# Kernel optimization log

Hardware: AMD Instinct MI355X
Metric: run time of the kernel (lower is better)

The kernel has to match this reference:

```python
import jax, jax.numpy as jnp
import numpy as np

LAM = 10.0          # lam_val from __init__ (cp.Constant)
N_ITERS = 100       # fixed FISTA iterations; converges to QP solution (kappa ~ 1+16*LAM)


def _dtd(v):
    """Apply D^T D where D is the (n-2, n) second-difference operator, along last axis."""
    d = v[..., 2:] - 2.0 * v[..., 1:-1] + v[..., :-2]            # D v, shape (..., n-2)
    pad = [(0, 0)] * (v.ndim - 1) + [(2, 2)]
    dp = jnp.pad(d, pad)                                          # zero-pad for adjoint
    return dp[..., 2:] - 2.0 * dp[..., 1:-1] + dp[..., :-2]      # D^T d, shape (..., n)


def _solve_rows(y):
    """Batched QP:  min ||y - x||^2 + LAM * ||diff(x, 2)||^2  s.t.  0 <= x <= y,
    solved independently along the last axis via projected accelerated gradient (FISTA).
    Hessian/2 = I + LAM * D^T D, lambda_max(D^T D) <= 16 -> Lipschitz L = 2*(1 + 16*LAM).
    """
    step = 1.0 / (2.0 * (1.0 + 16.0 * LAM))
    proj = lambda v: jnp.clip(v, 0.0, y)   # box projection onto [0, y]
    x0 = proj(y)

    def body(i, carry):
        x, z, t = carry
        g = 2.0 * (z - y) + (2.0 * LAM) * _dtd(z)
        x_new = proj(z - step * g)
        t_new = 0.5 * (1.0 + jnp.sqrt(1.0 + 4.0 * t * t))
        z_new = x_new + ((t - 1.0) / t_new) * (x_new - x)
        return (x_new, z_new, t_new)

    x, _, _ = jax.lax.fori_loop(0, N_ITERS, body, (x0, x0, jnp.float32(1.0)))
    return x


def setup_inputs() -> dict:
    key = jax.random.key(0)
    # Batch of images in [0,1] (like normalized MNIST); constraint 0 <= x <= y is feasible.
    data = jax.random.uniform(key, (32, 512, 512), dtype=jnp.float32)
    return {"data": data}


def reference(data):
    # Pass 1: denoise each row of each image.
    pass1 = _solve_rows(data)
    # Pass 2: the original call() transposes a numpy VIEW and writes in place, so its
    # "column" pass actually re-solves the SAME rows (with y = pass-1 output) and the
    # final transpose undoes itself. We replicate that exact math.
    pass2 = _solve_rows(pass1)
    b, h, w = pass2.shape
    return pass2.reshape(b, h, w, 1)
```

## Files before the change

kernel.cpp:

```cpp
#include <hip/hip_runtime.h>
#include <math.h>

#define ROW_N 512
#define N_ITERS 100
#define LAMBDA 10.0f

typedef float f2 __attribute__((ext_vector_type(2)));

__device__ __forceinline__ f2 splat(float s) { f2 r; r.x = s; r.y = s; return r; }
__device__ __forceinline__ f2 ffma(f2 a, f2 b, f2 c) {
    return __builtin_elementwise_fma(a, b, c);
}

__global__ void coef_kernel(float* __restrict__ coefs) {
    if (threadIdx.x == 0) {
        float t = 1.0f;
        for (int k = 0; k < N_ITERS; ++k) {
            float t_new = 0.5f * (1.0f + sqrtf(1.0f + 4.0f * t * t));
            coefs[k] = (t - 1.0f) / t_new;
            t = t_new;
        }
    }
}

template <bool USE_TABLE>
__global__ __launch_bounds__(256)
__attribute__((amdgpu_waves_per_eu(2, 8)))
void fista_kernel(
    const float* __restrict__ in, float* __restrict__ out,
    const float* __restrict__ coefs, int n_rows)
{
    const int pid  = (int)((blockIdx.x * 256u + threadIdx.x) >> 6);
    const int lane = (int)(threadIdx.x & 63u);
    const int n_pairs = (n_rows + 1) >> 1;
    if (pid >= n_pairs) return;

    const bool lane_lo = (lane == 0);
    const bool lane_hi = (lane == 63);

    const int r0 = pid * 2;
    const int r1 = (r0 + 1 < n_rows) ? r0 + 1 : r0;
    const float* rowA = in + (size_t)r0 * ROW_N + lane * 8;
    const float* rowB = in + (size_t)r1 * ROW_N + lane * 8;

    const float A = 1.0f / (1.0f + 16.0f * LAMBDA);
    const float B = LAMBDA / (1.0f + 16.0f * LAMBDA);
    const float C = 1.0f - A;
    const f2 Cv = splat(C), Av = splat(A), Bn = splat(-B), M2 = splat(-2.0f);
    const f2 Z2 = splat(0.0f);

    f2 y[8], ay[8], x[8], z[8];
    {
        const float4 a0 = *(const float4*)(rowA);
        const float4 a1 = *(const float4*)(rowA + 4);
        const float4 b0 = *(const float4*)(rowB);
        const float4 b1 = *(const float4*)(rowB + 4);
        y[0].x = a0.x; y[1].x = a0.y; y[2].x = a0.z; y[3].x = a0.w;
        y[4].x = a1.x; y[5].x = a1.y; y[6].x = a1.z; y[7].x = a1.w;
        y[0].y = b0.x; y[1].y = b0.y; y[2].y = b0.z; y[3].y = b0.w;
        y[4].y = b1.x; y[5].y = b1.y; y[6].y = b1.z; y[7].y = b1.w;
    }

    #pragma unroll 1
    for (int pass = 0; pass < 2; ++pass) {
        #pragma unroll
        for (int i = 0; i < 8; ++i) {
            ay[i] = Av * y[i];
            f2 x0;
            x0.x = fminf(fmaxf(y[i].x, 0.0f), y[i].x);
            x0.y = fminf(fmaxf(y[i].y, 0.0f), y[i].y);
            x[i] = x0;
            z[i] = x0;
        }

        f2 zm2, zm1, zp0, zp1;
        zm2.x = __shfl_up(z[6].x, 1);   zm2.y = __shfl_up(z[6].y, 1);
        zm1.x = __shfl_up(z[7].x, 1);   zm1.y = __shfl_up(z[7].y, 1);
        zp0.x = __shfl_down(z[0].x, 1); zp0.y = __shfl_down(z[0].y, 1);
        zp1.x = __shfl_down(z[1].x, 1); zp1.y = __shfl_down(z[1].y, 1);
        float coef, t = 1.0f;
        if (USE_TABLE) coef = coefs[0];
        else           coef = 0.0f;

        #pragma unroll 2
        for (int it = 0; it < N_ITERS; ++it) {
            float coef_next;
            if (USE_TABLE) {
                coef_next = coefs[it + 1 < N_ITERS ? it + 1 : 0];
            } else {
                float t_new = 0.5f + sqrtf(fmaf(t, t, 0.25f));
                coef_next = (t_new - 1.0f) / (0.5f + sqrtf(fmaf(t_new, t_new, 0.25f)));
                t = t_new;
            }

            const f2 cf = splat(coef);
            auto upd = [&](int i, f2 da, f2 db, f2 dc) {
                f2 dtd = ffma(M2, db, da + dc);
                f2 u = ffma(Cv, z[i], ay[i]);
                u = ffma(Bn, dtd, u);
                f2 xn;
                xn.x = __builtin_amdgcn_fmed3f(u.x, 0.0f, y[i].x);
                xn.y = __builtin_amdgcn_fmed3f(u.y, 0.0f, y[i].y);
                z[i] = ffma(cf, xn - x[i], xn);
                x[i] = xn;
            };

            f2 dd2 = ffma(M2, z[1], z[0] + z[2]);
            f2 dd3 = ffma(M2, z[2], z[1] + z[3]);
            f2 dd4 = ffma(M2, z[3], z[2] + z[4]);
            f2 dd5 = ffma(M2, z[4], z[3] + z[5]);
            f2 dd6 = ffma(M2, z[5], z[4] + z[6]);
            f2 dd7 = ffma(M2, z[6], z[5] + z[7]);

            upd(2, dd2, dd3, dd4);
            upd(3, dd3, dd4, dd5);
            upd(4, dd4, dd5, dd6);
            upd(5, dd5, dd6, dd7);

            f2 dd8 = ffma(M2, z[7], z[6] + zp0);
            f2 dd9 = ffma(M2, zp0, z[7] + zp1);
            if (lane_hi) { dd8 = Z2; dd9 = Z2; }

            upd(6, dd6, dd7, dd8);
            upd(7, dd7, dd8, dd9);

            f2 nzm2, nzm1;
            nzm2.x = __shfl_up(z[6].x, 1); nzm2.y = __shfl_up(z[6].y, 1);
            nzm1.x = __shfl_up(z[7].x, 1); nzm1.y = __shfl_up(z[7].y, 1);

            f2 dd0 = ffma(M2, zm1, zm2 + z[0]);
            f2 dd1 = ffma(M2, z[0], zm1 + z[1]);
            if (lane_lo) { dd0 = Z2; dd1 = Z2; }

            upd(0, dd0, dd1, dd2);
            upd(1, dd1, dd2, dd3);

            zp0.x = __shfl_down(z[0].x, 1); zp0.y = __shfl_down(z[0].y, 1);
            zp1.x = __shfl_down(z[1].x, 1); zp1.y = __shfl_down(z[1].y, 1);

            zm2 = nzm2; zm1 = nzm1;
            coef = coef_next;
        }

        #pragma unroll
        for (int i = 0; i < 8; ++i) y[i] = x[i];
    }

    float* orowA = out + (size_t)r0 * ROW_N + lane * 8;
    *(float4*)(orowA)     = make_float4(x[0].x, x[1].x, x[2].x, x[3].x);
    *(float4*)(orowA + 4) = make_float4(x[4].x, x[5].x, x[6].x, x[7].x);
    if (r1 > r0) {
        float* orowB = out + (size_t)r1 * ROW_N + lane * 8;
        *(float4*)(orowB)     = make_float4(x[0].y, x[1].y, x[2].y, x[3].y);
        *(float4*)(orowB + 4) = make_float4(x[4].y, x[5].y, x[6].y, x[7].y);
    }
}

extern "C" void kernel_launch(void* const* d_in, const int* in_sizes, int n_in,
                              void* d_out, int out_size, void* d_ws, size_t ws_size,
                              hipStream_t stream) {
    const float* in = (const float*)d_in[0];
    float* out = (float*)d_out;

    const int total   = in_sizes[0];
    const int n_rows  = total / ROW_N;
    const int n_pairs = (n_rows + 1) >> 1;
    const int waves_per_block = 4;
    const int blocks = (n_pairs + waves_per_block - 1) / waves_per_block;

    if (ws_size >= N_ITERS * sizeof(float)) {
        float* coefs = (float*)d_ws;
        coef_kernel<<<1, 64, 0, stream>>>(coefs);
        fista_kernel<true><<<blocks, 256, 0, stream>>>(in, out, coefs, n_rows);
    } else {
        fista_kernel<false><<<blocks, 256, 0, stream>>>(in, out, nullptr, n_rows);
    }
}
```

Measured before the change: 360.6 us.

## Expand DᵀD stencil into pentadiagonal FMA form and reorder shuffles for overlap

Rewrites each gradient step to apply DᵀD directly as a 5-point pentadiagonal stencil with precomputed coefficients (C-6B, 4B, -B), with boundary-lane coefficients chosen per lane instead of masking intermediate second differences. Edge elements are updated first so the cross-lane shuffles for the next iteration can be issued before the interior updates, hiding shuffle latency. The coefficient table is padded so the per-iteration index clamp can be dropped. The cost is a few extra per-lane constant registers; the reassociated stencil can also change floating-point rounding slightly.

```diff
diff --git a/kernel.cpp b/kernel.cpp
--- a/kernel.cpp
+++ b/kernel.cpp
@@ -3,6 +3,7 @@
 
 #define ROW_N 512
 #define N_ITERS 100
+#define CTAB_N (N_ITERS + 4)
 #define LAMBDA 10.0f
 
 typedef float f2 __attribute__((ext_vector_type(2)));
@@ -15,10 +16,14 @@
 __global__ void coef_kernel(float* __restrict__ coefs) {
     if (threadIdx.x == 0) {
         float t = 1.0f;
-        for (int k = 0; k < N_ITERS; ++k) {
-            float t_new = 0.5f * (1.0f + sqrtf(1.0f + 4.0f * t * t));
-            coefs[k] = (t - 1.0f) / t_new;
-            t = t_new;
+        float c = 0.0f;
+        for (int k = 0; k < CTAB_N; ++k) {
+            if (k < N_ITERS) {
+                float t_new = 0.5f * (1.0f + sqrtf(1.0f + 4.0f * t * t));
+                c = (t - 1.0f) / t_new;
+                t = t_new;
+            }
+            coefs[k] = c;
         }
     }
 }
@@ -46,8 +51,18 @@
     const float A = 1.0f / (1.0f + 16.0f * LAMBDA);
     const float B = LAMBDA / (1.0f + 16.0f * LAMBDA);
     const float C = 1.0f - A;
-    const f2 Cv = splat(C), Av = splat(A), Bn = splat(-B), M2 = splat(-2.0f);
+    const f2 Av = splat(A);
+    const f2 C6 = splat(C - 6.0f * B);
+    const f2 B4 = splat(4.0f * B);
+    const f2 Bm = splat(-B);
     const f2 Z2 = splat(0.0f);
+
+    const f2 cz0   = lane_lo ? splat(C - B)        : C6;
+    const f2 cz1   = lane_lo ? splat(C - 5.0f * B) : C6;
+    const f2 ca_lo = lane_lo ? splat(2.0f * B)     : B4;
+    const f2 cz6   = lane_hi ? splat(C - 5.0f * B) : C6;
+    const f2 cz7   = lane_hi ? splat(C - B)        : C6;
+    const f2 ca_hi = lane_hi ? splat(2.0f * B)     : B4;
 
     f2 y[8], ay[8], x[8], z[8];
     {
@@ -86,7 +101,7 @@
         for (int it = 0; it < N_ITERS; ++it) {
             float coef_next;
             if (USE_TABLE) {
-                coef_next = coefs[it + 1 < N_ITERS ? it + 1 : 0];
+                coef_next = coefs[it + 1];
             } else {
                 float t_new = 0.5f + sqrtf(fmaf(t, t, 0.25f));
                 coef_next = (t_new - 1.0f) / (0.5f + sqrtf(fmaf(t_new, t_new, 0.25f)));
@@ -94,10 +109,7 @@
             }
 
             const f2 cf = splat(coef);
-            auto upd = [&](int i, f2 da, f2 db, f2 dc) {
-                f2 dtd = ffma(M2, db, da + dc);
-                f2 u = ffma(Cv, z[i], ay[i]);
-                u = ffma(Bn, dtd, u);
+            auto fin = [&](int i, f2 u) {
                 f2 xn;
                 xn.x = __builtin_amdgcn_fmed3f(u.x, 0.0f, y[i].x);
                 xn.y = __builtin_amdgcn_fmed3f(u.y, 0.0f, y[i].y);
@@ -105,40 +117,66 @@
                 x[i] = xn;
             };
 
-            f2 dd2 = ffma(M2, z[1], z[0] + z[2]);
-            f2 dd3 = ffma(M2, z[2], z[1] + z[3]);
-            f2 dd4 = ffma(M2, z[3], z[2] + z[4]);
-            f2 dd5 = ffma(M2, z[4], z[3] + z[5]);
-            f2 dd6 = ffma(M2, z[5], z[4] + z[6]);
-            f2 dd7 = ffma(M2, z[6], z[5] + z[7]);
-
-            upd(2, dd2, dd3, dd4);
-            upd(3, dd3, dd4, dd5);
-            upd(4, dd4, dd5, dd6);
-            upd(5, dd5, dd6, dd7);
-
-            f2 dd8 = ffma(M2, z[7], z[6] + zp0);
-            f2 dd9 = ffma(M2, zp0, z[7] + zp1);
-            if (lane_hi) { dd8 = Z2; dd9 = Z2; }
-
-            upd(6, dd6, dd7, dd8);
-            upd(7, dd7, dd8, dd9);
-
+            if (lane_lo) { zm2 = Z2; zm1 = Z2; }
+            if (lane_hi) { zp0 = Z2; zp1 = Z2; }
+
+            f2 ta0 = zm1 + z[1];
+            f2 tb0 = zm2 + z[2];
+            f2 tb1 = zm1 + z[3];
+            f2 tb6 = z[4] + zp0;
+            f2 ta7 = z[6] + zp0;
+            f2 tb7 = z[5] + zp1;
+
+            f2 u0 = ffma(cz0, z[0], ay[0]);
+            u0 = ffma(ca_lo, ta0, u0);
+            u0 = ffma(Bm, tb0, u0);
+            f2 u1 = ffma(cz1, z[1], ay[1]);
+            u1 = ffma(ca_lo, z[0], u1);
+            u1 = ffma(B4, z[2], u1);
+            u1 = ffma(Bm, tb1, u1);
+            f2 u6 = ffma(cz6, z[6], ay[6]);
+            u6 = ffma(B4, z[5], u6);
+            u6 = ffma(ca_hi, z[7], u6);
+            u6 = ffma(Bm, tb6, u6);
+            f2 u7 = ffma(cz7, z[7], ay[7]);
+            u7 = ffma(ca_hi, ta7, u7);
+            u7 = ffma(Bm, tb7, u7);
+
+            f2 ta2 = z[1] + z[3], tb2 = z[0] + z[4];
+            f2 ta3 = z[2] + z[4], tb3 = z[1] + z[5];
+            f2 ta4 = z[3] + z[5], tb4 = z[2] + z[6];
+            f2 ta5 = z[4] + z[6], tb5 = z[3] + z[7];
+
+            fin(6, u6);
+            fin(7, u7);
             f2 nzm2, nzm1;
             nzm2.x = __shfl_up(z[6].x, 1); nzm2.y = __shfl_up(z[6].y, 1);
             nzm1.x = __shfl_up(z[7].x, 1); nzm1.y = __shfl_up(z[7].y, 1);
 
-            f2 dd0 = ffma(M2, zm1, zm2 + z[0]);
-            f2 dd1 = ffma(M2, z[0], zm1 + z[1]);
-            if (lane_lo) { dd0 = Z2; dd1 = Z2; }
-
-            upd(0, dd0, dd1, dd2);
-            upd(1, dd1, dd2, dd3);
-
-            zp0.x = __shfl_down(z[0].x, 1); zp0.y = __shfl_down(z[0].y, 1);
-            zp1.x = __shfl_down(z[1].x, 1); zp1.y = __shfl_down(z[1].y, 1);
-
-            zm2 = nzm2; zm1 = nzm1;
+            fin(0, u0);
+            fin(1, u1);
+            f2 nzp0, nzp1;
+            nzp0.x = __shfl_down(z[0].x, 1); nzp0.y = __shfl_down(z[0].y, 1);
+            nzp1.x = __shfl_down(z[1].x, 1); nzp1.y = __shfl_down(z[1].y, 1);
+
+            f2 u2 = ffma(C6, z[2], ay[2]);
+            u2 = ffma(B4, ta2, u2);
+            u2 = ffma(Bm, tb2, u2);
+            fin(2, u2);
+            f2 u3 = ffma(C6, z[3], ay[3]);
+            u3 = ffma(B4, ta3, u3);
+            u3 = ffma(Bm, tb3, u3);
+            fin(3, u3);
+            f2 u4 = ffma(C6, z[4], ay[4]);
+            u4 = ffma(B4, ta4, u4);
+            u4 = ffma(Bm, tb4, u4);
+            fin(4, u4);
+            f2 u5 = ffma(C6, z[5], ay[5]);
+            u5 = ffma(B4, ta5, u5);
+            u5 = ffma(Bm, tb5, u5);
+            fin(5, u5);
+
+            zm2 = nzm2; zm1 = nzm1; zp0 = nzp0; zp1 = nzp1;
             coef = coef_next;
         }
 
@@ -168,7 +206,7 @@
     const int waves_per_block = 4;
     const int blocks = (n_pairs + waves_per_block - 1) / waves_per_block;
 
-    if (ws_size >= N_ITERS * sizeof(float)) {
+    if (ws_size >= CTAB_N * sizeof(float)) {
         float* coefs = (float*)d_ws;
         coef_kernel<<<1, 64, 0, stream>>>(coefs);
         fista_kernel<true><<<blocks, 256, 0, stream>>>(in, out, coefs, n_rows);
```

Result: no change. 363.4 us (+0.8%).
